# Kernel optimization log

Measured on AMD Instinct MI355X. Metric: run time of the kernel, lower is better.

Reference implementation:

```python
import jax, jax.numpy as jnp
import numpy as np

N_NODES = 50000
N_EDGES = 800000
IN_DIM = 96
HID_DIM = 96


def setup_inputs() -> dict:
    key = jax.random.key(0)
    ks = jax.random.split(key, 8)
    inputs = jax.random.normal(ks[0], (N_NODES, IN_DIM), dtype=jnp.float32)
    factor = jax.random.uniform(ks[1], (N_EDGES, 1), dtype=jnp.float32)
    src = jax.random.randint(ks[2], (N_EDGES,), 0, N_NODES, dtype=jnp.int32)
    dst = jax.random.randint(ks[3], (N_EDGES,), 0, N_NODES, dtype=jnp.int32)
    # Linear params (torch nn.Linear: y = x @ W.T + b), uniform(-1/sqrt(fan_in), ..)
    s1 = 1.0 / np.sqrt(IN_DIM)
    s2 = 1.0 / np.sqrt(HID_DIM)
    W1 = jax.random.uniform(ks[4], (HID_DIM, IN_DIM), minval=-s1, maxval=s1, dtype=jnp.float32)
    b1 = jax.random.uniform(ks[5], (HID_DIM,), minval=-s1, maxval=s1, dtype=jnp.float32)
    W2 = jax.random.uniform(ks[6], (IN_DIM, HID_DIM), minval=-s2, maxval=s2, dtype=jnp.float32)
    b2 = jax.random.uniform(ks[7], (IN_DIM,), minval=-s2, maxval=s2, dtype=jnp.float32)
    return {"inputs": inputs, "W1": W1, "b1": b1, "W2": W2, "b2": b2,
            "factor": factor, "src": src, "dst": dst}


def _propagate(feat, factor, src, dst, n_nodes):
    # message = h[src] * edge_factor ; reduce = sum at dst
    msg = feat[src] * factor                       # [E, D]
    return jax.ops.segment_sum(msg, dst, num_segments=n_nodes)


def reference(inputs, W1, b1, W2, b2, factor, src, dst):
    n = inputs.shape[0]
    # in-degree norm: deg^{-1/2}, clamped at 1
    deg = jax.ops.segment_sum(jnp.ones((src.shape[0],), inputs.dtype), dst,
                              num_segments=n)
    norm = jnp.maximum(deg, 1.0) ** -0.5           # [N]
    norm = norm[:, None]                           # [N, 1]

    feat = (inputs @ W1.T + b1) * norm             # [N, H]
    h = jnp.tanh(_propagate(feat, factor, src, dst, n))

    feat = (h @ W2.T + b2) * norm                  # [N, D]
    h = jnp.tanh(_propagate(feat, factor, src, dst, n))

    # dgl.mean_nodes over a single graph -> [1, D]; unsqueeze(-1) -> [1, D, 1]
    pooled = jnp.mean(h, axis=0, keepdims=True)[..., None]
    return jnp.tanh(pooled)
```

## Files before the change

kernel.cpp:

```cpp
#include <hip/hip_runtime.h>
#include <math.h>
#include <type_traits>

#define N_NODES 50000
#define N_EDGES 800000
#define DIM 96
#define BCH 12
#define SCAN_BLK 256
#define NBLK ((N_NODES + SCAN_BLK - 1) / SCAN_BLK)
#define GBLK 512
#define NPB 42
#define NBG ((N_NODES + NPB - 1) / NPB)
#define CAP 768
#define R1_ROWS 24
#define R1_BLOCKS ((NBG + R1_ROWS - 1) / R1_ROWS)
#define SC_PASSES 4
#define SC_WIN ((N_NODES + SC_PASSES - 1) / SC_PASSES)
#define F8_SCALE 16.0f
#define F8_INV   0.0625f
#define TILE_SH 104

typedef short v8s __attribute__((ext_vector_type(8)));
typedef float v4f __attribute__((ext_vector_type(4)));
typedef float v2f __attribute__((ext_vector_type(2)));

__device__ __forceinline__ unsigned short f2bf(float f) {
    unsigned int u = __float_as_uint(f);
    u += 0x7FFFu + ((u >> 16) & 1u);
    return (unsigned short)(u >> 16);
}
__device__ __forceinline__ unsigned int pack2bf(float lo, float hi) {
    return (unsigned int)f2bf(lo) | ((unsigned int)f2bf(hi) << 16);
}

__device__ __forceinline__ float fast_tanh(float x) {
    float ax = fabsf(x);
    float t = __expf(-2.0f * ax);
    float r = (1.0f - t) / (1.0f + t);
    return copysignf(r, x);
}

__device__ __forceinline__ void accf8(float* a, uint2 v, float f) {
    v2f p0 = __builtin_amdgcn_cvt_pk_f32_fp8(v.x, false);
    v2f p1 = __builtin_amdgcn_cvt_pk_f32_fp8(v.x, true);
    v2f p2 = __builtin_amdgcn_cvt_pk_f32_fp8(v.y, false);
    v2f p3 = __builtin_amdgcn_cvt_pk_f32_fp8(v.y, true);
    a[0] += p0.x * f; a[1] += p0.y * f;
    a[2] += p1.x * f; a[3] += p1.y * f;
    a[4] += p2.x * f; a[5] += p2.y * f;
    a[6] += p3.x * f; a[7] += p3.y * f;
}

union U4S8 { uint4 u; v8s s; };


__global__ void count_deg(const int* __restrict__ dst, int* __restrict__ deg,
                          int* __restrict__ rank) {
    int e = blockIdx.x * blockDim.x + threadIdx.x;
    if (e < N_EDGES) rank[e] = atomicAdd(&deg[dst[e]], 1);
}

__global__ void deg_partials(const int* __restrict__ deg, float* __restrict__ norm,
                             int* __restrict__ partials) {
    int b = blockIdx.x, t = threadIdx.x;
    int n = b * SCAN_BLK + t;
    int v = 0;
    if (n < N_NODES) {
        v = deg[n];
        norm[n] = rsqrtf(fmaxf((float)v, 1.0f));
    }
    int s = v;
#pragma unroll
    for (int off = 32; off > 0; off >>= 1) s += __shfl_down(s, off, 64);
    __shared__ int ws_[4];
    if ((t & 63) == 0) ws_[t >> 6] = s;
    __syncthreads();
    if (t == 0) partials[b] = ws_[0] + ws_[1] + ws_[2] + ws_[3];
}

__global__ void scan_partials(const int* __restrict__ partials, int* __restrict__ pprefix) {
    __shared__ int sm[SCAN_BLK];
    int t = threadIdx.x;
    int v = (t < NBLK) ? partials[t] : 0;
    sm[t] = v;
    __syncthreads();
    for (int off = 1; off < SCAN_BLK; off <<= 1) {
        int u = (t >= off) ? sm[t - off] : 0;
        __syncthreads();
        sm[t] += u;
        __syncthreads();
    }
    if (t < NBLK) pprefix[t] = sm[t] - v;
}

__global__ void make_offsets(const int* __restrict__ deg, const int* __restrict__ pprefix,
                             int* __restrict__ offs) {
    __shared__ int sm[SCAN_BLK];
    int b = blockIdx.x, t = threadIdx.x;
    int idx = b * SCAN_BLK + t;
    int v = (idx < N_NODES) ? deg[idx] : 0;
    sm[t] = v;
    __syncthreads();
    for (int off = 1; off < SCAN_BLK; off <<= 1) {
        int u = (t >= off) ? sm[t - off] : 0;
        __syncthreads();
        sm[t] += u;
        __syncthreads();
    }
    if (idx < N_NODES) offs[idx] = pprefix[b] + sm[t] - v;
    if (b == 0 && t == 0) offs[N_NODES] = N_EDGES;
}

__global__ void scatter_edges(const int* __restrict__ src, const int* __restrict__ dst,
                              const float* __restrict__ factor, const int* __restrict__ rank,
                              const int* __restrict__ offs, int2* __restrict__ entries) {
    int tid0 = blockIdx.x * blockDim.x + threadIdx.x;
    int stride = gridDim.x * blockDim.x;
#pragma unroll 1
    for (int pass = 0; pass < SC_PASSES; ++pass) {
        int lo = pass * SC_WIN;
        int hi = min(lo + SC_WIN, N_NODES);
#pragma unroll 1
        for (int e = tid0; e < N_EDGES; e += stride) {
            int d = dst[e];
            if (d >= lo && d < hi) {
                int pos = offs[d] + rank[e];
                entries[pos] = make_int2(src[e], __float_as_int(factor[e]));
            }
        }
    }
}


__global__ void swizzle_W(const float* __restrict__ W, uint4* __restrict__ bsw) {
    int idx = blockIdx.x * blockDim.x + threadIdx.x;
    if (idx >= 18 * 64) return;
    int t = idx >> 6, lane = idx & 63;
    int kt = t / 6, jt = t % 6;
    int quad = lane >> 4, l16 = lane & 15;
    const float4* wp = (const float4*)(W + (size_t)(jt * 16 + l16) * DIM + kt * 32 + quad * 8);
    float4 w0 = wp[0], w1 = wp[1];
    bsw[idx] = make_uint4(pack2bf(w0.x, w0.y), pack2bf(w0.z, w0.w),
                          pack2bf(w1.x, w1.y), pack2bf(w1.z, w1.w));
}


template <typename T>
__global__ __launch_bounds__(256) void gemm_mfma(const T* __restrict__ X,
                                                 const uint4* __restrict__ bsw,
                                                 const float* __restrict__ bias,
                                                 const float* __restrict__ norm,
                                                 unsigned char* __restrict__ out) {
    int tid = threadIdx.x;
    int wave = tid >> 6, lane = tid & 63;
    int quad = lane >> 4, l16 = lane & 15;
    int n0 = blockIdx.x * 64 + wave * 16;
    int node = n0 + l16;
    int rowc = min(node, N_NODES - 1);

    uint4 bfr[18];
#pragma unroll
    for (int t = 0; t < 18; ++t) bfr[t] = bsw[t * 64 + lane];

    v4f acc[6];
#pragma unroll
    for (int jt = 0; jt < 6; ++jt) acc[jt] = (v4f)(0.0f);

#pragma unroll
    for (int kt = 0; kt < 3; ++kt) {
        U4S8 x;
        if constexpr (std::is_same_v<T, float>) {
            const float4* xp = (const float4*)(X + (size_t)rowc * DIM + kt * 32 + quad * 8);
            float4 x0 = xp[0], x1 = xp[1];
            x.u = make_uint4(pack2bf(x0.x, x0.y), pack2bf(x0.z, x0.w),
                             pack2bf(x1.x, x1.y), pack2bf(x1.z, x1.w));
        } else {
            x.u = *(const uint4*)(X + (size_t)rowc * DIM + kt * 32 + quad * 8);
        }
#pragma unroll
        for (int jt = 0; jt < 6; ++jt) {
            U4S8 w; w.u = bfr[kt * 6 + jt];
            acc[jt] = __builtin_amdgcn_mfma_f32_16x16x32_bf16(w.s, x.s, acc[jt], 0, 0, 0);
        }
    }

    if (node < N_NODES) {
        float nm = norm[node] * F8_SCALE;
#pragma unroll
        for (int jt = 0; jt < 6; ++jt) {
            float4 bj = *(const float4*)(bias + jt * 16 + quad * 4);
            float v0 = (acc[jt][0] + bj.x) * nm;
            float v1 = (acc[jt][1] + bj.y) * nm;
            float v2 = (acc[jt][2] + bj.z) * nm;
            float v3 = (acc[jt][3] + bj.w) * nm;
            unsigned int w = (unsigned int)__builtin_amdgcn_cvt_pk_fp8_f32(v0, v1, 0, false);
            w = (unsigned int)__builtin_amdgcn_cvt_pk_fp8_f32(v2, v3, (int)w, true);
            *(unsigned int*)(out + (size_t)node * DIM + jt * 16 + quad * 4) = w;
        }
    }
}


__global__ __launch_bounds__(GBLK) void gather_fuse(
        const unsigned char* __restrict__ feat,
        const int* __restrict__ offs,
        const int2* __restrict__ entries,
        const uint4* __restrict__ bsw2,
        const float* __restrict__ bias2,
        const float* __restrict__ norm,
        unsigned char* __restrict__ feat2) {
    __shared__ int2 ents[CAP];
    __shared__ __align__(16) unsigned short h1s[48 * TILE_SH];
    __shared__ int sh_base, sh_cnt;
    int tid = threadIdx.x;
    for (int i = tid; i < 48 * TILE_SH / 2; i += GBLK) ((unsigned int*)h1s)[i] = 0u;
    int n0 = blockIdx.x * NPB;
    int n1 = min(n0 + NPB, N_NODES);
    if (tid == 0) { sh_base = offs[n0]; sh_cnt = offs[n1] - sh_base; }
    __syncthreads();
    int base = sh_base, cnt = sh_cnt;

    int nl = tid / BCH;
    int c  = tid - nl * BCH;
    int n  = n0 + nl;
    bool active = (tid < NPB * BCH) && (n < N_NODES);
    int lb = 0, le = 0;
    if (active) { lb = offs[n] - base; le = offs[n + 1] - base; }

    float a0[8], a1[8];
#pragma unroll
    for (int i = 0; i < 8; ++i) { a0[i] = 0.f; a1[i] = 0.f; }

    for (int tb = 0; tb < cnt; tb += CAP) {
        int tcnt = min(cnt - tb, CAP);
        if (tb) __syncthreads();
        for (int i = tid; i < tcnt; i += GBLK) ents[i] = entries[base + tb + i];
        __syncthreads();
        int s = max(lb - tb, 0), e = min(le - tb, tcnt);
        int p = s;
        for (; p + 7 < e; p += 8) {
            int2 q0 = ents[p + 0], q1 = ents[p + 1], q2 = ents[p + 2], q3 = ents[p + 3];
            int2 q4 = ents[p + 4], q5 = ents[p + 5], q6 = ents[p + 6], q7 = ents[p + 7];
            uint2 v0 = *((const uint2*)(feat + (size_t)q0.x * DIM) + c);
            uint2 v1 = *((const uint2*)(feat + (size_t)q1.x * DIM) + c);
            uint2 v2 = *((const uint2*)(feat + (size_t)q2.x * DIM) + c);
            uint2 v3 = *((const uint2*)(feat + (size_t)q3.x * DIM) + c);
            uint2 v4 = *((const uint2*)(feat + (size_t)q4.x * DIM) + c);
            uint2 v5 = *((const uint2*)(feat + (size_t)q5.x * DIM) + c);
            uint2 v6 = *((const uint2*)(feat + (size_t)q6.x * DIM) + c);
            uint2 v7 = *((const uint2*)(feat + (size_t)q7.x * DIM) + c);
            accf8(a0, v0, __int_as_float(q0.y));
            accf8(a1, v1, __int_as_float(q1.y));
            accf8(a0, v2, __int_as_float(q2.y));
            accf8(a1, v3, __int_as_float(q3.y));
            accf8(a0, v4, __int_as_float(q4.y));
            accf8(a1, v5, __int_as_float(q5.y));
            accf8(a0, v6, __int_as_float(q6.y));
            accf8(a1, v7, __int_as_float(q7.y));
        }
        for (; p + 3 < e; p += 4) {
            int2 q0 = ents[p], q1 = ents[p + 1], q2 = ents[p + 2], q3 = ents[p + 3];
            uint2 v0 = *((const uint2*)(feat + (size_t)q0.x * DIM) + c);
            uint2 v1 = *((const uint2*)(feat + (size_t)q1.x * DIM) + c);
            uint2 v2 = *((const uint2*)(feat + (size_t)q2.x * DIM) + c);
            uint2 v3 = *((const uint2*)(feat + (size_t)q3.x * DIM) + c);
            accf8(a0, v0, __int_as_float(q0.y));
            accf8(a1, v1, __int_as_float(q1.y));
            accf8(a0, v2, __int_as_float(q2.y));
            accf8(a1, v3, __int_as_float(q3.y));
        }
        for (; p < e; ++p) {
            int2 q0 = ents[p];
            uint2 v0 = *((const uint2*)(feat + (size_t)q0.x * DIM) + c);
            accf8(a0, v0, __int_as_float(q0.y));
        }
    }

    if (active) {
#pragma unroll
        for (int i = 0; i < 8; ++i) a0[i] = fast_tanh((a0[i] + a1[i]) * F8_INV);
        uint4 o;
        o.x = pack2bf(a0[0], a0[1]);
        o.y = pack2bf(a0[2], a0[3]);
        o.z = pack2bf(a0[4], a0[5]);
        o.w = pack2bf(a0[6], a0[7]);
        *(uint4*)&h1s[nl * TILE_SH + c * 8] = o;
    }
    __syncthreads();

    int wave = tid >> 6, lane = tid & 63;
    if (wave < 3) {
        int quad = lane >> 4, l16 = lane & 15;
        uint4 bfr[18];
#pragma unroll
        for (int t = 0; t < 18; ++t) bfr[t] = bsw2[t * 64 + lane];
        v4f acc[6];
#pragma unroll
        for (int jt = 0; jt < 6; ++jt) acc[jt] = (v4f)(0.0f);
#pragma unroll
        for (int kt = 0; kt < 3; ++kt) {
            U4S8 x;
            x.u = *(const uint4*)&h1s[(wave * 16 + l16) * TILE_SH + kt * 32 + quad * 8];
#pragma unroll
            for (int jt = 0; jt < 6; ++jt) {
                U4S8 w; w.u = bfr[kt * 6 + jt];
                acc[jt] = __builtin_amdgcn_mfma_f32_16x16x32_bf16(w.s, x.s, acc[jt], 0, 0, 0);
            }
        }
        int local = wave * 16 + l16;
        int node = n0 + local;
        if (local < n1 - n0) {
            float nm = norm[node] * F8_SCALE;
#pragma unroll
            for (int jt = 0; jt < 6; ++jt) {
                float4 bj = *(const float4*)(bias2 + jt * 16 + quad * 4);
                float v0 = (acc[jt][0] + bj.x) * nm;
                float v1 = (acc[jt][1] + bj.y) * nm;
                float v2 = (acc[jt][2] + bj.z) * nm;
                float v3 = (acc[jt][3] + bj.w) * nm;
                unsigned int w = (unsigned int)__builtin_amdgcn_cvt_pk_fp8_f32(v0, v1, 0, false);
                w = (unsigned int)__builtin_amdgcn_cvt_pk_fp8_f32(v2, v3, (int)w, true);
                *(unsigned int*)(feat2 + (size_t)node * DIM + jt * 16 + quad * 4) = w;
            }
        }
    }
}


__global__ __launch_bounds__(GBLK) void gather_pool(
        const unsigned char* __restrict__ feat,
        const int* __restrict__ offs,
        const int2* __restrict__ entries,
        float* __restrict__ partials) {
    __shared__ int2 ents[CAP];
    __shared__ float pool[DIM];
    __shared__ int sh_base, sh_cnt;
    int tid = threadIdx.x;
    int n0 = blockIdx.x * NPB;
    int n1 = min(n0 + NPB, N_NODES);
    if (tid < DIM) pool[tid] = 0.f;
    if (tid == 0) { sh_base = offs[n0]; sh_cnt = offs[n1] - sh_base; }
    __syncthreads();
    int base = sh_base, cnt = sh_cnt;

    int nl = tid / BCH;
    int c  = tid - nl * BCH;
    int n  = n0 + nl;
    bool active = (tid < NPB * BCH) && (n < N_NODES);
    int lb = 0, le = 0;
    if (active) { lb = offs[n] - base; le = offs[n + 1] - base; }

    float a0[8], a1[8];
#pragma unroll
    for (int i = 0; i < 8; ++i) { a0[i] = 0.f; a1[i] = 0.f; }

    for (int tb = 0; tb < cnt; tb += CAP) {
        int tcnt = min(cnt - tb, CAP);
        if (tb) __syncthreads();
        for (int i = tid; i < tcnt; i += GBLK) ents[i] = entries[base + tb + i];
        __syncthreads();
        int s = max(lb - tb, 0), e = min(le - tb, tcnt);
        int p = s;
        for (; p + 7 < e; p += 8) {
            int2 q0 = ents[p + 0], q1 = ents[p + 1], q2 = ents[p + 2], q3 = ents[p + 3];
            int2 q4 = ents[p + 4], q5 = ents[p + 5], q6 = ents[p + 6], q7 = ents[p + 7];
            uint2 v0 = *((const uint2*)(feat + (size_t)q0.x * DIM) + c);
            uint2 v1 = *((const uint2*)(feat + (size_t)q1.x * DIM) + c);
            uint2 v2 = *((const uint2*)(feat + (size_t)q2.x * DIM) + c);
            uint2 v3 = *((const uint2*)(feat + (size_t)q3.x * DIM) + c);
            uint2 v4 = *((const uint2*)(feat + (size_t)q4.x * DIM) + c);
            uint2 v5 = *((const uint2*)(feat + (size_t)q5.x * DIM) + c);
            uint2 v6 = *((const uint2*)(feat + (size_t)q6.x * DIM) + c);
            uint2 v7 = *((const uint2*)(feat + (size_t)q7.x * DIM) + c);
            accf8(a0, v0, __int_as_float(q0.y));
            accf8(a1, v1, __int_as_float(q1.y));
            accf8(a0, v2, __int_as_float(q2.y));
            accf8(a1, v3, __int_as_float(q3.y));
            accf8(a0, v4, __int_as_float(q4.y));
            accf8(a1, v5, __int_as_float(q5.y));
            accf8(a0, v6, __int_as_float(q6.y));
            accf8(a1, v7, __int_as_float(q7.y));
        }
        for (; p + 3 < e; p += 4) {
            int2 q0 = ents[p], q1 = ents[p + 1], q2 = ents[p + 2], q3 = ents[p + 3];
            uint2 v0 = *((const uint2*)(feat + (size_t)q0.x * DIM) + c);
            uint2 v1 = *((const uint2*)(feat + (size_t)q1.x * DIM) + c);
            uint2 v2 = *((const uint2*)(feat + (size_t)q2.x * DIM) + c);
            uint2 v3 = *((const uint2*)(feat + (size_t)q3.x * DIM) + c);
            accf8(a0, v0, __int_as_float(q0.y));
            accf8(a1, v1, __int_as_float(q1.y));
            accf8(a0, v2, __int_as_float(q2.y));
            accf8(a1, v3, __int_as_float(q3.y));
        }
        for (; p < e; ++p) {
            int2 q0 = ents[p];
            uint2 v0 = *((const uint2*)(feat + (size_t)q0.x * DIM) + c);
            accf8(a0, v0, __int_as_float(q0.y));
        }
    }

#pragma unroll
    for (int i = 0; i < 8; ++i) a0[i] = fast_tanh((a0[i] + a1[i]) * F8_INV);
    if (active) {
#pragma unroll
        for (int i = 0; i < 8; ++i) atomicAdd(&pool[c * 8 + i], a0[i]);
    }
    __syncthreads();
    if (tid < DIM) partials[(size_t)blockIdx.x * DIM + tid] = pool[tid];
}


__global__ void reduce_stage1(const float* __restrict__ poolpart, float* __restrict__ stage1) {
    __shared__ float pool[DIM];
    int b = blockIdx.x, t = threadIdx.x;
    if (t < DIM) pool[t] = 0.f;
    __syncthreads();
    const int base = b * R1_ROWS * DIM;
    float loc = 0.f;
    int lastc = -1;
    for (int i = t; i < R1_ROWS * DIM; i += 256) {
        int gi = base + i;
        if (gi < NBG * DIM) {
            int col = i % DIM;
            if (col != lastc) {
                if (lastc >= 0) atomicAdd(&pool[lastc], loc);
                lastc = col; loc = 0.f;
            }
            loc += poolpart[gi];
        }
    }
    if (lastc >= 0) atomicAdd(&pool[lastc], loc);
    __syncthreads();
    if (t < DIM) stage1[b * DIM + t] = pool[t];
}

__global__ void reduce_stage2(const float* __restrict__ stage1, float* __restrict__ out) {
    __shared__ float sm[960];
    int t = threadIdx.x;
    int col = t % DIM, slice = t / DIM;
    float s = 0.f;
    for (int k = slice; k < R1_BLOCKS; k += 10) s += stage1[k * DIM + col];
    sm[t] = s;
    __syncthreads();
    if (t < DIM) {
        float tot = 0.f;
#pragma unroll
        for (int i = 0; i < 10; ++i) tot += sm[i * DIM + t];
        out[t] = tanhf(tot * (1.0f / N_NODES));
    }
}


extern "C" void kernel_launch(void* const* d_in, const int* in_sizes, int n_in,
                              void* d_out, int out_size, void* d_ws, size_t ws_size,
                              hipStream_t stream) {
    const float* inputs = (const float*)d_in[0];
    const float* W1     = (const float*)d_in[1];
    const float* b1     = (const float*)d_in[2];
    const float* W2     = (const float*)d_in[3];
    const float* b2     = (const float*)d_in[4];
    const float* factor = (const float*)d_in[5];
    const int*   src    = (const int*)d_in[6];
    const int*   dst    = (const int*)d_in[7];
    float* out = (float*)d_out;

    char* ws = (char*)d_ws;
    int*            deg      = (int*)(ws + 0);
    int*            rank     = (int*)(ws + 262144);
    int*            offs     = (int*)(ws + 3670016);
    float*          norm     = (float*)(ws + 3932160);
    int*            partials = (int*)(ws + 4194304);
    int*            pprefix  = (int*)(ws + 4196352);
    int2*           entries  = (int2*)(ws + 4456448);
    unsigned char*  bufA     = (unsigned char*)(ws + 11534336);
    unsigned char*  bufB     = (unsigned char*)(ws + 16777216);
    float*          poolpart = (float*)(ws + 26738688);
    float*          stage1   = (float*)(ws + 27787264);
    uint4*          bsw1     = (uint4*)(ws + 27836416);
    uint4*          bsw2     = (uint4*)(ws + 27856896);

    swizzle_W<<<5, 256, 0, stream>>>(W1, bsw1);
    swizzle_W<<<5, 256, 0, stream>>>(W2, bsw2);

    hipMemsetAsync(deg, 0, N_NODES * sizeof(int), stream);
    count_deg<<<(N_EDGES + 255) / 256, 256, 0, stream>>>(dst, deg, rank);
    deg_partials<<<NBLK, SCAN_BLK, 0, stream>>>(deg, norm, partials);
    scan_partials<<<1, SCAN_BLK, 0, stream>>>(partials, pprefix);
    make_offsets<<<NBLK, SCAN_BLK, 0, stream>>>(deg, pprefix, offs);
    scatter_edges<<<2048, 256, 0, stream>>>(src, dst, factor, rank, offs, entries);

    const int GEMM_BLOCKS = (N_NODES + 63) / 64;

    gemm_mfma<float><<<GEMM_BLOCKS, 256, 0, stream>>>(inputs, bsw1, b1, norm, bufA);

    gather_fuse<<<NBG, GBLK, 0, stream>>>(bufA, offs, entries, bsw2, b2, norm, bufB);

    gather_pool<<<NBG, GBLK, 0, stream>>>(bufB, offs, entries, poolpart);

    reduce_stage1<<<R1_BLOCKS, 256, 0, stream>>>(poolpart, stage1);
    reduce_stage2<<<1, 960, 0, stream>>>(stage1, out);
}
```

Baseline: 224.2 us.

## Merge small kernels to cut launch count and co-run GEMM with edge scatter

Folds the weight swizzles into the degree-count kernel and the partial-sum scan into make_offsets, with each block redundantly scanning the block partials. The first GEMM and the edge scatter now run in one launch on disjoint block ranges, so they can overlap. The two-stage final reduction becomes a single-block float4 reduction. The aim is to remove launch and serialization gaps between many tiny kernels, at the cost of redundant scan work per block and a single-block final reduction.

```diff
diff --git a/kernel.cpp b/kernel.cpp
--- a/kernel.cpp
+++ b/kernel.cpp
@@ -12,13 +12,13 @@
 #define NPB 42
 #define NBG ((N_NODES + NPB - 1) / NPB)
 #define CAP 768
-#define R1_ROWS 24
-#define R1_BLOCKS ((NBG + R1_ROWS - 1) / R1_ROWS)
 #define SC_PASSES 4
 #define SC_WIN ((N_NODES + SC_PASSES - 1) / SC_PASSES)
 #define F8_SCALE 16.0f
 #define F8_INV   0.0625f
 #define TILE_SH 104
+#define GEMM_BLOCKS ((N_NODES + 63) / 64)
+#define SCAT_BLOCKS 2048
 
 typedef short v8s __attribute__((ext_vector_type(8)));
 typedef float v4f __attribute__((ext_vector_type(4)));
@@ -54,9 +54,23 @@
 union U4S8 { uint4 u; v8s s; };
 
 
-__global__ void count_deg(const int* __restrict__ dst, int* __restrict__ deg,
-                          int* __restrict__ rank) {
+__global__ void count_deg_swz(const int* __restrict__ dst, int* __restrict__ deg,
+                              int* __restrict__ rank,
+                              const float* __restrict__ W1, const float* __restrict__ W2,
+                              uint4* __restrict__ bsw1, uint4* __restrict__ bsw2) {
     int e = blockIdx.x * blockDim.x + threadIdx.x;
+    if (e < 2 * 1152) {
+        int w = e / 1152, idx = e % 1152;
+        const float* W = w ? W2 : W1;
+        uint4* bsw = w ? bsw2 : bsw1;
+        int t18 = idx >> 6, lane = idx & 63;
+        int kt = t18 / 6, jt = t18 % 6;
+        int quad = lane >> 4, l16 = lane & 15;
+        const float4* wp = (const float4*)(W + (size_t)(jt * 16 + l16) * DIM + kt * 32 + quad * 8);
+        float4 w0 = wp[0], w1 = wp[1];
+        bsw[idx] = make_uint4(pack2bf(w0.x, w0.y), pack2bf(w0.z, w0.w),
+                              pack2bf(w1.x, w1.y), pack2bf(w1.z, w1.w));
+    }
     if (e < N_EDGES) rank[e] = atomicAdd(&deg[dst[e]], 1);
 }
 
@@ -78,25 +92,20 @@
     if (t == 0) partials[b] = ws_[0] + ws_[1] + ws_[2] + ws_[3];
 }
 
-__global__ void scan_partials(const int* __restrict__ partials, int* __restrict__ pprefix) {
-    __shared__ int sm[SCAN_BLK];
-    int t = threadIdx.x;
-    int v = (t < NBLK) ? partials[t] : 0;
-    sm[t] = v;
-    __syncthreads();
-    for (int off = 1; off < SCAN_BLK; off <<= 1) {
-        int u = (t >= off) ? sm[t - off] : 0;
-        __syncthreads();
-        sm[t] += u;
-        __syncthreads();
-    }
-    if (t < NBLK) pprefix[t] = sm[t] - v;
-}
-
-__global__ void make_offsets(const int* __restrict__ deg, const int* __restrict__ pprefix,
+__global__ void make_offsets(const int* __restrict__ deg, const int* __restrict__ partials,
                              int* __restrict__ offs) {
     __shared__ int sm[SCAN_BLK];
+    __shared__ int sp[SCAN_BLK];
     int b = blockIdx.x, t = threadIdx.x;
+    sp[t] = (t < NBLK) ? partials[t] : 0;
+    __syncthreads();
+    for (int off = 1; off < SCAN_BLK; off <<= 1) {
+        int u = (t >= off) ? sp[t - off] : 0;
+        __syncthreads();
+        sp[t] += u;
+        __syncthreads();
+    }
+    int ppfx = (b > 0) ? sp[b - 1] : 0;
     int idx = b * SCAN_BLK + t;
     int v = (idx < N_NODES) ? deg[idx] : 0;
     sm[t] = v;
@@ -107,95 +116,77 @@
         sm[t] += u;
         __syncthreads();
     }
-    if (idx < N_NODES) offs[idx] = pprefix[b] + sm[t] - v;
+    if (idx < N_NODES) offs[idx] = ppfx + sm[t] - v;
     if (b == 0 && t == 0) offs[N_NODES] = N_EDGES;
 }
 
-__global__ void scatter_edges(const int* __restrict__ src, const int* __restrict__ dst,
-                              const float* __restrict__ factor, const int* __restrict__ rank,
-                              const int* __restrict__ offs, int2* __restrict__ entries) {
-    int tid0 = blockIdx.x * blockDim.x + threadIdx.x;
-    int stride = gridDim.x * blockDim.x;
-#pragma unroll 1
-    for (int pass = 0; pass < SC_PASSES; ++pass) {
-        int lo = pass * SC_WIN;
-        int hi = min(lo + SC_WIN, N_NODES);
-#pragma unroll 1
-        for (int e = tid0; e < N_EDGES; e += stride) {
-            int d = dst[e];
-            if (d >= lo && d < hi) {
-                int pos = offs[d] + rank[e];
-                entries[pos] = make_int2(src[e], __float_as_int(factor[e]));
-            }
-        }
-    }
-}
-
-
-__global__ void swizzle_W(const float* __restrict__ W, uint4* __restrict__ bsw) {
-    int idx = blockIdx.x * blockDim.x + threadIdx.x;
-    if (idx >= 18 * 64) return;
-    int t = idx >> 6, lane = idx & 63;
-    int kt = t / 6, jt = t % 6;
-    int quad = lane >> 4, l16 = lane & 15;
-    const float4* wp = (const float4*)(W + (size_t)(jt * 16 + l16) * DIM + kt * 32 + quad * 8);
-    float4 w0 = wp[0], w1 = wp[1];
-    bsw[idx] = make_uint4(pack2bf(w0.x, w0.y), pack2bf(w0.z, w0.w),
-                          pack2bf(w1.x, w1.y), pack2bf(w1.z, w1.w));
-}
-
-
-template <typename T>
-__global__ __launch_bounds__(256) void gemm_mfma(const T* __restrict__ X,
-                                                 const uint4* __restrict__ bsw,
-                                                 const float* __restrict__ bias,
-                                                 const float* __restrict__ norm,
-                                                 unsigned char* __restrict__ out) {
-    int tid = threadIdx.x;
-    int wave = tid >> 6, lane = tid & 63;
-    int quad = lane >> 4, l16 = lane & 15;
-    int n0 = blockIdx.x * 64 + wave * 16;
-    int node = n0 + l16;
-    int rowc = min(node, N_NODES - 1);
-
-    uint4 bfr[18];
-#pragma unroll
-    for (int t = 0; t < 18; ++t) bfr[t] = bsw[t * 64 + lane];
-
-    v4f acc[6];
-#pragma unroll
-    for (int jt = 0; jt < 6; ++jt) acc[jt] = (v4f)(0.0f);
-
-#pragma unroll
-    for (int kt = 0; kt < 3; ++kt) {
-        U4S8 x;
-        if constexpr (std::is_same_v<T, float>) {
+
+__global__ __launch_bounds__(256) void gemm1_scatter(
+        const float* __restrict__ X, const uint4* __restrict__ bsw,
+        const float* __restrict__ bias, const float* __restrict__ norm,
+        unsigned char* __restrict__ outF,
+        const int* __restrict__ src, const int* __restrict__ dst,
+        const float* __restrict__ factor, const int* __restrict__ rank,
+        const int* __restrict__ offs, int2* __restrict__ entries) {
+    if (blockIdx.x < GEMM_BLOCKS) {
+        int tid = threadIdx.x;
+        int wave = tid >> 6, lane = tid & 63;
+        int quad = lane >> 4, l16 = lane & 15;
+        int n0 = blockIdx.x * 64 + wave * 16;
+        int node = n0 + l16;
+        int rowc = min(node, N_NODES - 1);
+
+        uint4 bfr[18];
+#pragma unroll
+        for (int t = 0; t < 18; ++t) bfr[t] = bsw[t * 64 + lane];
+
+        v4f acc[6];
+#pragma unroll
+        for (int jt = 0; jt < 6; ++jt) acc[jt] = (v4f)(0.0f);
+
+#pragma unroll
+        for (int kt = 0; kt < 3; ++kt) {
+            U4S8 x;
             const float4* xp = (const float4*)(X + (size_t)rowc * DIM + kt * 32 + quad * 8);
             float4 x0 = xp[0], x1 = xp[1];
             x.u = make_uint4(pack2bf(x0.x, x0.y), pack2bf(x0.z, x0.w),
                              pack2bf(x1.x, x1.y), pack2bf(x1.z, x1.w));
-        } else {
-            x.u = *(const uint4*)(X + (size_t)rowc * DIM + kt * 32 + quad * 8);
-        }
-#pragma unroll
-        for (int jt = 0; jt < 6; ++jt) {
-            U4S8 w; w.u = bfr[kt * 6 + jt];
-            acc[jt] = __builtin_amdgcn_mfma_f32_16x16x32_bf16(w.s, x.s, acc[jt], 0, 0, 0);
-        }
-    }
-
-    if (node < N_NODES) {
-        float nm = norm[node] * F8_SCALE;
-#pragma unroll
-        for (int jt = 0; jt < 6; ++jt) {
-            float4 bj = *(const float4*)(bias + jt * 16 + quad * 4);
-            float v0 = (acc[jt][0] + bj.x) * nm;
-            float v1 = (acc[jt][1] + bj.y) * nm;
-            float v2 = (acc[jt][2] + bj.z) * nm;
-            float v3 = (acc[jt][3] + bj.w) * nm;
-            unsigned int w = (unsigned int)__builtin_amdgcn_cvt_pk_fp8_f32(v0, v1, 0, false);
-            w = (unsigned int)__builtin_amdgcn_cvt_pk_fp8_f32(v2, v3, (int)w, true);
-            *(unsigned int*)(out + (size_t)node * DIM + jt * 16 + quad * 4) = w;
+#pragma unroll
+            for (int jt = 0; jt < 6; ++jt) {
+                U4S8 w; w.u = bfr[kt * 6 + jt];
+                acc[jt] = __builtin_amdgcn_mfma_f32_16x16x32_bf16(w.s, x.s, acc[jt], 0, 0, 0);
+            }
+        }
+
+        if (node < N_NODES) {
+            float nm = norm[node] * F8_SCALE;
+#pragma unroll
+            for (int jt = 0; jt < 6; ++jt) {
+                float4 bj = *(const float4*)(bias + jt * 16 + quad * 4);
+                float v0 = (acc[jt][0] + bj.x) * nm;
+                float v1 = (acc[jt][1] + bj.y) * nm;
+                float v2 = (acc[jt][2] + bj.z) * nm;
+                float v3 = (acc[jt][3] + bj.w) * nm;
+                unsigned int w = (unsigned int)__builtin_amdgcn_cvt_pk_fp8_f32(v0, v1, 0, false);
+                w = (unsigned int)__builtin_amdgcn_cvt_pk_fp8_f32(v2, v3, (int)w, true);
+                *(unsigned int*)(outF + (size_t)node * DIM + jt * 16 + quad * 4) = w;
+            }
+        }
+    } else {
+        int tid0 = (blockIdx.x - GEMM_BLOCKS) * 256 + threadIdx.x;
+        int stride = (gridDim.x - GEMM_BLOCKS) * 256;
+#pragma unroll 1
+        for (int pass = 0; pass < SC_PASSES; ++pass) {
+            int lo = pass * SC_WIN;
+            int hi = min(lo + SC_WIN, N_NODES);
+#pragma unroll 1
+            for (int e = tid0; e < N_EDGES; e += stride) {
+                int d = dst[e];
+                if (d >= lo && d < hi) {
+                    int pos = offs[d] + rank[e];
+                    entries[pos] = make_int2(src[e], __float_as_int(factor[e]));
+                }
+            }
         }
     }
 }
@@ -410,43 +401,28 @@
 }
 
 
-__global__ void reduce_stage1(const float* __restrict__ poolpart, float* __restrict__ stage1) {
-    __shared__ float pool[DIM];
-    int b = blockIdx.x, t = threadIdx.x;
-    if (t < DIM) pool[t] = 0.f;
-    __syncthreads();
-    const int base = b * R1_ROWS * DIM;
-    float loc = 0.f;
-    int lastc = -1;
-    for (int i = t; i < R1_ROWS * DIM; i += 256) {
-        int gi = base + i;
-        if (gi < NBG * DIM) {
-            int col = i % DIM;
-            if (col != lastc) {
-                if (lastc >= 0) atomicAdd(&pool[lastc], loc);
-                lastc = col; loc = 0.f;
-            }
-            loc += poolpart[gi];
-        }
-    }
-    if (lastc >= 0) atomicAdd(&pool[lastc], loc);
-    __syncthreads();
-    if (t < DIM) stage1[b * DIM + t] = pool[t];
-}
-
-__global__ void reduce_stage2(const float* __restrict__ stage1, float* __restrict__ out) {
-    __shared__ float sm[960];
+__global__ void reduce_one(const float* __restrict__ poolpart, float* __restrict__ out) {
+    __shared__ float4 sm[960];
     int t = threadIdx.x;
-    int col = t % DIM, slice = t / DIM;
-    float s = 0.f;
-    for (int k = slice; k < R1_BLOCKS; k += 10) s += stage1[k * DIM + col];
+    int c4 = t % 24, slice = t / 24;
+    float4 s = make_float4(0.f, 0.f, 0.f, 0.f);
+    for (int k = slice; k < NBG; k += 40) {
+        float4 v = *(const float4*)(poolpart + (size_t)k * DIM + c4 * 4);
+        s.x += v.x; s.y += v.y; s.z += v.z; s.w += v.w;
+    }
     sm[t] = s;
     __syncthreads();
-    if (t < DIM) {
-        float tot = 0.f;
-#pragma unroll
-        for (int i = 0; i < 10; ++i) tot += sm[i * DIM + t];
-        out[t] = tanhf(tot * (1.0f / N_NODES));
+    if (t < 24) {
+        float4 tot = make_float4(0.f, 0.f, 0.f, 0.f);
+        for (int i = 0; i < 40; ++i) {
+            float4 v = sm[i * 24 + t];
+            tot.x += v.x; tot.y += v.y; tot.z += v.z; tot.w += v.w;
+        }
+        const float inv = 1.0f / N_NODES;
+        out[t * 4 + 0] = tanhf(tot.x * inv);
+        out[t * 4 + 1] = tanhf(tot.y * inv);
+        out[t * 4 + 2] = tanhf(tot.z * inv);
+        out[t * 4 + 3] = tanhf(tot.w * inv);
     }
 }
 
@@ -470,33 +446,25 @@
     int*            offs     = (int*)(ws + 3670016);
     float*          norm     = (float*)(ws + 3932160);
     int*            partials = (int*)(ws + 4194304);
-    int*            pprefix  = (int*)(ws + 4196352);
     int2*           entries  = (int2*)(ws + 4456448);
     unsigned char*  bufA     = (unsigned char*)(ws + 11534336);
     unsigned char*  bufB     = (unsigned char*)(ws + 16777216);
     float*          poolpart = (float*)(ws + 26738688);
-    float*          stage1   = (float*)(ws + 27787264);
     uint4*          bsw1     = (uint4*)(ws + 27836416);
     uint4*          bsw2     = (uint4*)(ws + 27856896);
 
-    swizzle_W<<<5, 256, 0, stream>>>(W1, bsw1);
-    swizzle_W<<<5, 256, 0, stream>>>(W2, bsw2);
-
     hipMemsetAsync(deg, 0, N_NODES * sizeof(int), stream);
-    count_deg<<<(N_EDGES + 255) / 256, 256, 0, stream>>>(dst, deg, rank);
+    count_deg_swz<<<(N_EDGES + 255) / 256, 256, 0, stream>>>(dst, deg, rank,
+                                                             W1, W2, bsw1, bsw2);
     deg_partials<<<NBLK, SCAN_BLK, 0, stream>>>(deg, norm, partials);
-    scan_partials<<<1, SCAN_BLK, 0, stream>>>(partials, pprefix);
-    make_offsets<<<NBLK, SCAN_BLK, 0, stream>>>(deg, pprefix, offs);
-    scatter_edges<<<2048, 256, 0, stream>>>(src, dst, factor, rank, offs, entries);
-
-    const int GEMM_BLOCKS = (N_NODES + 63) / 64;
-
-    gemm_mfma<float><<<GEMM_BLOCKS, 256, 0, stream>>>(inputs, bsw1, b1, norm, bufA);
+    make_offsets<<<NBLK, SCAN_BLK, 0, stream>>>(deg, partials, offs);
+
+    gemm1_scatter<<<GEMM_BLOCKS + SCAT_BLOCKS, 256, 0, stream>>>(
+        inputs, bsw1, b1, norm, bufA, src, dst, factor, rank, offs, entries);
 
     gather_fuse<<<NBG, GBLK, 0, stream>>>(bufA, offs, entries, bsw2, b2, norm, bufB);
 
     gather_pool<<<NBG, GBLK, 0, stream>>>(bufB, offs, entries, poolpart);
 
-    reduce_stage1<<<R1_BLOCKS, 256, 0, stream>>>(poolpart, stage1);
-    reduce_stage2<<<1, 960, 0, stream>>>(stage1, out);
-}
+    reduce_one<<<1, 960, 0, stream>>>(poolpart, out);
+}
```

New measurement: 224.5 us. Within noise of the previous version (+0.1%).
